# Optimization experiments

Hardware: AMD Instinct MI355X
Metric: run time of the kernel (lower is better)

Reference implementation:

```python
import jax, jax.numpy as jnp
import numpy as np

B, N, F_IN = 4, 8000, 256
D_DIST = 128   # distance_dim
DFF = 128      # hidden width of both FFNs
BIN_SIZE = 500
NBINS = N // BIN_SIZE  # 16
K = 8          # num_neighbors
DIST_MULT = 0.1
MAX_NUM_BINS = 200


def setup_inputs() -> dict:
    key = jax.random.key(0)
    ks = jax.random.split(key, 8)
    s = 0.05
    return {
        "inputs": jax.random.normal(ks[0], (B, N, F_IN), jnp.float32),
        "enc_w1": jax.random.normal(ks[1], (F_IN, DFF), jnp.float32) * s,
        "enc_b1": jnp.zeros((DFF,), jnp.float32),
        "enc_w2": jax.random.normal(ks[2], (DFF, D_DIST), jnp.float32) * s,
        "enc_b2": jnp.zeros((D_DIST,), jnp.float32),
        "edge_w1": jax.random.normal(ks[3], (2 * F_IN + 1, DFF), jnp.float32) * s,
        "edge_b1": jnp.zeros((DFF,), jnp.float32),
        "edge_w2": jax.random.normal(ks[4], (DFF, 1), jnp.float32) * s,
        "edge_b2": jnp.zeros((1,), jnp.float32),
        "rot": jax.random.normal(ks[5], (D_DIST, MAX_NUM_BINS // 2), jnp.float32) * 0.05,
    }


def _per_batch(points, rot):
    # points: [N, D_DIST]. LSH bucketing via random rotations.
    mul = points @ rot[:, : NBINS // 2]                 # [N, NBINS//2]
    cmul = jnp.concatenate([mul, -mul], axis=-1)        # [N, NBINS]
    bin_idx = jnp.argmax(cmul, axis=-1)
    bins_split = jnp.argsort(bin_idx).astype(jnp.int32).reshape(NBINS, BIN_SIZE)
    parts = points[bins_split]                          # [NBINS, BIN_SIZE, D]
    # per-bin pairwise gaussian kernel
    na = jnp.sum(parts * parts, axis=-1)                # [NBINS, BIN_SIZE]
    d2 = na[:, :, None] - 2.0 * jnp.einsum('bnd,bmd->bnm', parts, parts) + na[:, None, :]
    dm = jnp.exp(-DIST_MULT * jnp.sqrt(jnp.maximum(d2, 1e-6)))  # [NBINS, BS, BS]
    vals, idx = jax.lax.top_k(dm, K)                    # [NBINS, BS, K]
    dst = jax.vmap(lambda b, i: b[i])(bins_split, idx)  # map in-bin idx -> global
    src = jnp.broadcast_to(bins_split[:, :, None], dst.shape)
    return src.reshape(-1), dst.reshape(-1), vals.reshape(-1), bins_split


def reference(inputs, enc_w1, enc_b1, enc_w2, enc_b2,
              edge_w1, edge_b1, edge_w2, edge_b2, rot):
    # point encoding FFN: Dense(128, elu) -> Dense(distance_dim)
    pe = jax.nn.elu(inputs @ enc_w1 + enc_b1) @ enc_w2 + enc_b2  # [B, N, D_DIST]
    src, dst, vals, bins_split = jax.vmap(_per_batch, in_axes=(0, None))(pe, rot)
    bidx = jnp.broadcast_to(jnp.arange(B, dtype=jnp.int32)[:, None], src.shape)
    src = src.reshape(-1)
    dst = dst.reshape(-1)
    vals = vals.reshape(-1)
    bidx = bidx.reshape(-1)
    # tf.sparse.reorder: canonical row-major ordering (no duplicates: top-k
    # indices are distinct per row and src is unique per neighbor slot)
    order = jnp.lexsort((dst, src, bidx))
    bidx, src, dst, vals = bidx[order], src[order], dst[order], vals[order]
    # edge network on gathered endpoint features + kernel value
    x1 = inputs[bidx, src]                               # [E, F_IN]
    x2 = inputs[bidx, dst]
    e = jnp.concatenate([x1, x2, vals[:, None]], axis=-1)  # [E, 2*F_IN+1]
    edge_vals = jax.nn.sigmoid(jax.nn.elu(e @ edge_w1 + edge_b1) @ edge_w2 + edge_b2)[:, 0]
    indices = jnp.stack([bidx, src, dst], axis=-1)       # [E, 3] sparse indices
    return indices, edge_vals, bins_split
```

## Files before the change

### kernel.cpp

```cpp
#include <hip/hip_runtime.h>
#include <math.h>

#define BB 4
#define NN 8000
#define FIN 256
#define DD 128
#define NB 16
#define BS 500
#define KK 8
#define RPB 32
#define CHUNKS (NN/RPB)
#define ETOT (BB*NN*KK)

__global__ __launch_bounds__(128) void k_encode(
    const float* __restrict__ x, const float* __restrict__ w1, const float* __restrict__ b1,
    const float* __restrict__ w2, const float* __restrict__ b2, const float* __restrict__ rot,
    float* __restrict__ pe, int* __restrict__ bin_idx, int* __restrict__ localrank,
    int* __restrict__ chunkhist)
{
  __shared__ float xs[RPB*FIN];
  __shared__ float hs[RPB*DD];
  __shared__ float ps[RPB*129];
  __shared__ float ms[RPB*9];
  __shared__ int   bl[RPB];
  const int t = threadIdx.x;
  const int blk = blockIdx.x;
  const int b = blk / CHUNKS;
  const int chunk = blk % CHUNKS;
  const int row0 = chunk * RPB;

  const float4* xg4 = (const float4*)(x + ((size_t)b*NN + row0)*FIN);
  float4* xs4 = (float4*)xs;
  #pragma unroll
  for (int i=0;i<16;i++) xs4[t + i*128] = xg4[t + i*128];
  __syncthreads();

  float acc[RPB];
  { float bias = b1[t];
    #pragma unroll
    for (int r=0;r<RPB;r++) acc[r]=bias; }
  for (int k=0;k<FIN;k++){
    float w = w1[k*DD + t];
    #pragma unroll
    for (int r=0;r<RPB;r++) acc[r] = fmaf(xs[r*FIN+k], w, acc[r]);
  }
  #pragma unroll
  for (int r=0;r<RPB;r++){ float v=acc[r]; hs[r*DD+t] = v>0.f ? v : expm1f(v); }
  __syncthreads();

  { float bias = b2[t];
    #pragma unroll
    for (int r=0;r<RPB;r++) acc[r]=bias; }
  for (int k=0;k<DD;k++){
    float w = w2[k*DD + t];
    #pragma unroll
    for (int r=0;r<RPB;r++) acc[r] = fmaf(hs[r*DD+k], w, acc[r]);
  }
  #pragma unroll
  for (int r=0;r<RPB;r++){
    float v = acc[r];
    pe[((size_t)b*NN + row0 + r)*DD + t] = v;
    ps[r*129+t] = v;
  }
  __syncthreads();

  { const int r = t>>2, m0 = t&3;
    float s0=0.f, s1=0.f;
    for (int k=0;k<DD;k++){
      float p = ps[r*129+k];
      s0 = fmaf(p, rot[k*100+m0],   s0);
      s1 = fmaf(p, rot[k*100+m0+4], s1);
    }
    ms[r*9+m0]=s0; ms[r*9+m0+4]=s1; }
  __syncthreads();

  if (t<RPB){
    float best = ms[t*9+0]; int bi=0;
    #pragma unroll
    for (int m=1;m<16;m++){
      float v = (m<8)? ms[t*9+m] : -ms[t*9+(m-8)];
      if (v>best){best=v;bi=m;}
    }
    bl[t]=bi;
    bin_idx[b*NN+row0+t]=bi;
  }
  __syncthreads();
  if (t<RPB){
    int myb=bl[t]; int rk=0;
    for (int r2=0;r2<t;r2++) rk += (bl[r2]==myb) ? 1 : 0;
    localrank[b*NN+row0+t]=rk;
  }
  if (t<NB){
    int cnt=0;
    #pragma unroll
    for (int r2=0;r2<RPB;r2++) cnt += (bl[r2]==t) ? 1 : 0;
    chunkhist[(b*CHUNKS+chunk)*NB + t] = cnt;
  }
}

__global__ __launch_bounds__(128) void k_tables(
    const float* __restrict__ x, const float* __restrict__ ew1,
    float* __restrict__ A, float* __restrict__ Bv)
{
  __shared__ float xs[RPB*FIN];
  const int t=threadIdx.x, blk=blockIdx.x;
  const int b=blk/CHUNKS, chunk=blk%CHUNKS, row0=chunk*RPB;
  const float4* xg4=(const float4*)(x+((size_t)b*NN+row0)*FIN);
  float4* xs4=(float4*)xs;
  #pragma unroll
  for (int i=0;i<16;i++) xs4[t+i*128]=xg4[t+i*128];
  __syncthreads();
  float aA[RPB], aB[RPB];
  #pragma unroll
  for (int r=0;r<RPB;r++){aA[r]=0.f;aB[r]=0.f;}
  for (int k=0;k<FIN;k++){
    float wa=ew1[k*DD+t], wb=ew1[(FIN+k)*DD+t];
    #pragma unroll
    for (int r=0;r<RPB;r++){
      float xv=xs[r*FIN+k];
      aA[r]=fmaf(xv,wa,aA[r]); aB[r]=fmaf(xv,wb,aB[r]);
    }
  }
  #pragma unroll
  for (int r=0;r<RPB;r++){
    A [((size_t)b*NN+row0+r)*DD+t]=aA[r];
    Bv[((size_t)b*NN+row0+r)*DD+t]=aB[r];
  }
}

__global__ __launch_bounds__(256) void k_scan_scatter(
    const int* __restrict__ bin_idx, const int* __restrict__ localrank,
    const int* __restrict__ chunkhist, int* __restrict__ bs, float* __restrict__ out_bins)
{
  const int b=blockIdx.x, t=threadIdx.x;
  __shared__ int cbase_s[CHUNKS*NB];
  __shared__ int tot[NB], start[NB];
  if (t<NB){
    int s=0;
    for (int c=0;c<CHUNKS;c++) s+=chunkhist[(b*CHUNKS+c)*NB+t];
    tot[t]=s;
  }
  __syncthreads();
  if (t==0){
    int run=0;
    for (int m=0;m<NB;m++){ start[m]=run; run+=tot[m]; }
  }
  __syncthreads();
  if (t<NB){
    int run=start[t];
    for (int c=0;c<CHUNKS;c++){
      cbase_s[c*NB+t]=run;
      run+=chunkhist[(b*CHUNKS+c)*NB+t];
    }
  }
  __syncthreads();
  for (int row=t; row<NN; row+=256){
    int gi=b*NN+row;
    int chunk=row>>5;
    int bi=bin_idx[gi];
    int pos=cbase_s[chunk*NB+bi]+localrank[gi];
    bs[b*NN+pos]=row;
    out_bins[b*NN+pos]=(float)row;
  }
}

__global__ __launch_bounds__(256) void k_nn(
    const float* __restrict__ pe, const int* __restrict__ bs,
    float* __restrict__ out_idx, int* __restrict__ e_dst, float* __restrict__ e_val)
{
  __shared__ float RT[64*129];
  __shared__ float CT[64*129];
  __shared__ float na_all[512];
  __shared__ int   bsl[BS];
  const int t=threadIdx.x;
  const int blk=blockIdx.x;
  const int rt=blk&7, bin=(blk>>3)&15, b=blk>>7;

  for (int i=t;i<BS;i+=256) bsl[i]=bs[b*NN + bin*BS + i];
  __syncthreads();

  for (int i=t;i<BS;i+=256){
    const float* pr = pe + ((size_t)b*NN + bsl[i])*DD;
    float s=0.f;
    for (int k=0;k<DD;k+=4){
      float4 v=*(const float4*)(pr+k);
      s=fmaf(v.x,v.x,s); s=fmaf(v.y,v.y,s); s=fmaf(v.z,v.z,s); s=fmaf(v.w,v.w,s);
    }
    na_all[i]=s;
  }

  const int r0=rt*64;
  const int nr=min(64, BS-r0);
  { const int lr=t>>5, c4=t&31;
    #pragma unroll
    for (int pass=0;pass<8;pass++){
      int r=pass*8+lr;
      float4 v=make_float4(0.f,0.f,0.f,0.f);
      if (r<nr) v=*(const float4*)(pe + ((size_t)b*NN + bsl[r0+r])*DD + c4*4);
      float* d=&RT[r*129 + c4*4];
      d[0]=v.x;d[1]=v.y;d[2]=v.z;d[3]=v.w;
    } }

  float tv[4][8]; int tix[4][8];
  #pragma unroll
  for (int i=0;i<4;i++){
    #pragma unroll
    for (int s=0;s<8;s++){ tv[i][s]=-1e30f; tix[i][s]=0; } }

  const int tr_=t>>4, tc_=t&15;

  for (int ct=0; ct<8; ++ct){
    __syncthreads();
    const int c0=ct*64;
    const int nc=min(64, BS-c0);
    { const int lr=t>>5, c4=t&31;
      #pragma unroll
      for (int pass=0;pass<8;pass++){
        int c=pass*8+lr;
        float4 v=make_float4(0.f,0.f,0.f,0.f);
        if (c<nc) v=*(const float4*)(pe + ((size_t)b*NN + bsl[c0+c])*DD + c4*4);
        float* d=&CT[c*129 + c4*4];
        d[0]=v.x;d[1]=v.y;d[2]=v.z;d[3]=v.w;
      } }
    __syncthreads();

    float accm[4][4];
    #pragma unroll
    for (int i=0;i<4;i++){
      #pragma unroll
      for (int j=0;j<4;j++) accm[i][j]=0.f; }
    for (int k2=0;k2<DD;k2++){
      float av[4], bv[4];
      #pragma unroll
      for (int i=0;i<4;i++) av[i]=RT[(tr_*4+i)*129+k2];
      #pragma unroll
      for (int j=0;j<4;j++) bv[j]=CT[(tc_*4+j)*129+k2];
      #pragma unroll
      for (int i=0;i<4;i++){
        #pragma unroll
        for (int j=0;j<4;j++) accm[i][j]=fmaf(av[i],bv[j],accm[i][j]); }
    }

    float nrow[4], ncol[4];
    #pragma unroll
    for (int i=0;i<4;i++) nrow[i]=na_all[r0+tr_*4+i];
    #pragma unroll
    for (int j=0;j<4;j++) ncol[j]=na_all[c0+tc_*4+j];

    #pragma unroll
    for (int i=0;i<4;i++){
      #pragma unroll
      for (int j=0;j<4;j++){
        float t1=nrow[i]-2.f*accm[i][j];
        float d2v=t1+ncol[j];
        float dm=expf(-0.1f*sqrtf(fmaxf(d2v,1e-6f)));
        int c=c0+tc_*4+j;
        if (c<BS && dm>tv[i][7]){
          tv[i][7]=dm; tix[i][7]=c;
          #pragma unroll
          for (int q=7;q>0;q--){
            if (tv[i][q]>tv[i][q-1]){
              float tf=tv[i][q];tv[i][q]=tv[i][q-1];tv[i][q-1]=tf;
              int   td=tix[i][q];tix[i][q]=tix[i][q-1];tix[i][q-1]=td;
            }
          }
        }
      }
    }
  }

  __syncthreads();
  #pragma unroll
  for (int i=0;i<4;i++){
    const int row=tr_*4+i;
    #pragma unroll
    for (int s=0;s<8;s++){
      RT[row*129 + tc_*8 + s]=tv[i][s];
      CT[row*129 + tc_*8 + s]=__int_as_float(tix[i][s]);
    }
  }
  __syncthreads();

  if (t<nr){
    float mv[8]; int mi[8];
    #pragma unroll
    for (int s=0;s<8;s++){ mv[s]=-1e30f; mi[s]=0; }
    for (int p=0;p<128;p++){
      float v=RT[t*129+p]; int c=__float_as_int(CT[t*129+p]);
      if (v>mv[7] || (v==mv[7] && c<mi[7])){
        mv[7]=v; mi[7]=c;
        #pragma unroll
        for (int q=7;q>0;q--){
          bool sw=(mv[q]>mv[q-1]) || (mv[q]==mv[q-1] && mi[q]<mi[q-1]);
          if (sw){
            float tf=mv[q];mv[q]=mv[q-1];mv[q-1]=tf;
            int   td=mi[q];mi[q]=mi[q-1];mi[q-1]=td;
          }
        }
      }
    }
    const int src=bsl[r0+t];
    int dsts[KK]; float vv[KK];
    #pragma unroll
    for (int k2=0;k2<KK;k2++){ dsts[k2]=bsl[mi[k2]]; vv[k2]=mv[k2]; }
    #define CSWAP(a_,b_) { if (dsts[a_]>dsts[b_]){ int td=dsts[a_];dsts[a_]=dsts[b_];dsts[b_]=td; float tf=vv[a_];vv[a_]=vv[b_];vv[b_]=tf; } }
    CSWAP(0,1) CSWAP(2,3) CSWAP(4,5) CSWAP(6,7)
    CSWAP(0,2) CSWAP(1,3) CSWAP(4,6) CSWAP(5,7)
    CSWAP(1,2) CSWAP(5,6)
    CSWAP(0,4) CSWAP(1,5) CSWAP(2,6) CSWAP(3,7)
    CSWAP(2,4) CSWAP(3,5)
    CSWAP(1,2) CSWAP(3,4) CSWAP(5,6)
    #undef CSWAP
    size_t e0=((size_t)b*NN + src)*KK;
    #pragma unroll
    for (int k2=0;k2<KK;k2++){
      out_idx[3*(e0+k2)+0]=(float)b;
      out_idx[3*(e0+k2)+1]=(float)src;
      out_idx[3*(e0+k2)+2]=(float)dsts[k2];
      e_dst[e0+k2]=dsts[k2];
      e_val[e0+k2]=vv[k2];
    }
  }
}

__global__ __launch_bounds__(256) void k_edge(
    const float* __restrict__ A, const float* __restrict__ Bv,
    const float* __restrict__ ew1, const float* __restrict__ eb1,
    const float* __restrict__ ew2, const float* __restrict__ eb2,
    const int* __restrict__ e_dst, const float* __restrict__ e_val,
    float* __restrict__ out_vals)
{
  const int wid = (int)((blockIdx.x*256u+threadIdx.x)>>6);
  const int lane = threadIdx.x&63;
  if (wid >= BB*NN) return;
  const int b = wid / NN;
  const float2 a2  = *(const float2*)(A   + (size_t)wid*DD + lane*2);
  const float2 wc  = *(const float2*)(ew1 + (size_t)512*DD + lane*2);
  const float2 bb1 = *(const float2*)(eb1 + lane*2);
  const float2 w2v = *(const float2*)(ew2 + lane*2);
  const float  b2s = eb2[0];
  const size_t e0 = (size_t)wid*KK;
  #pragma unroll
  for (int k=0;k<KK;k++){
    int dst = e_dst[e0+k];
    float val = e_val[e0+k];
    const float2 bv = *(const float2*)(Bv + ((size_t)b*NN+dst)*DD + lane*2);
    float h0 = a2.x + bv.x + val*wc.x + bb1.x;  h0 = h0>0.f ? h0 : expm1f(h0);
    float h1 = a2.y + bv.y + val*wc.y + bb1.y;  h1 = h1>0.f ? h1 : expm1f(h1);
    float s = h0*w2v.x + h1*w2v.y;
    #pragma unroll
    for (int off=32; off; off>>=1) s += __shfl_xor(s, off);
    if (lane==k) out_vals[e0+k] = 1.f/(1.f+expf(-(s+b2s)));
  }
}

extern "C" void kernel_launch(void* const* d_in, const int* in_sizes, int n_in,
                              void* d_out, int out_size, void* d_ws, size_t ws_size,
                              hipStream_t stream)
{
  const float* x    = (const float*)d_in[0];
  const float* ew1v = (const float*)d_in[1];
  const float* eb1v = (const float*)d_in[2];
  const float* ew2v = (const float*)d_in[3];
  const float* eb2v = (const float*)d_in[4];
  const float* gw1  = (const float*)d_in[5];
  const float* gb1  = (const float*)d_in[6];
  const float* gw2  = (const float*)d_in[7];
  const float* gb2  = (const float*)d_in[8];
  const float* rot  = (const float*)d_in[9];

  char* w = (char*)d_ws;
  float* pe   = (float*)w;  w += (size_t)BB*NN*DD*4;
  float* Atab = (float*)w;  w += (size_t)BB*NN*DD*4;
  float* Btab = (float*)w;  w += (size_t)BB*NN*DD*4;
  int*   bin_idx   = (int*)w; w += (size_t)BB*NN*4;
  int*   localrank = (int*)w; w += (size_t)BB*NN*4;
  int*   chunkhist = (int*)w; w += (size_t)BB*CHUNKS*NB*4;
  int*   bs        = (int*)w; w += (size_t)BB*NN*4;
  int*   e_dst     = (int*)w; w += (size_t)ETOT*4;
  float* e_val     = (float*)w; w += (size_t)ETOT*4;

  float* out_idx  = (float*)d_out;
  float* out_vals = out_idx + (size_t)ETOT*3;
  float* out_bins = out_vals + ETOT;

  k_encode<<<dim3(BB*CHUNKS), dim3(128), 0, stream>>>(
      x, ew1v, eb1v, ew2v, eb2v, rot, pe, bin_idx, localrank, chunkhist);
  k_tables<<<dim3(BB*CHUNKS), dim3(128), 0, stream>>>(x, gw1, Atab, Btab);
  k_scan_scatter<<<dim3(BB), dim3(256), 0, stream>>>(
      bin_idx, localrank, chunkhist, bs, out_bins);
  k_nn<<<dim3(BB*NB*8), dim3(256), 0, stream>>>(pe, bs, out_idx, e_dst, e_val);
  k_edge<<<dim3(BB*NN/4), dim3(256), 0, stream>>>(
      Atab, Btab, gw1, gb1, gw2, gb2, e_dst, e_val, out_vals);
}
```

Baseline: 585.2 us.

## Register-tile encoder and table GEMMs; vectorize swizzled LDS reads in kNN

The encoder and edge-table kernels now use a 4x8 register tile per thread, with weights staged through shared memory in 32-row slabs. This replaces the old scheme of one column per thread with 32 rows of accumulators and a scalar global weight load on every k. The kNN distance kernel pads its tiles to a stride of 132 and reads float4 vectors from LDS, using an XOR swizzle on the column tile to avoid bank conflicts. The aim is to cut LDS and global load instructions per FMA, at the cost of more syncthreads and more shared memory per block, which may lower occupancy.

```diff
diff --git a/kernel.cpp b/kernel.cpp
--- a/kernel.cpp
+++ b/kernel.cpp
@@ -18,56 +18,126 @@
     float* __restrict__ pe, int* __restrict__ bin_idx, int* __restrict__ localrank,
     int* __restrict__ chunkhist)
 {
-  __shared__ float xs[RPB*FIN];
-  __shared__ float hs[RPB*DD];
-  __shared__ float ps[RPB*129];
+  __shared__ float xs[RPB*260];
+  __shared__ float ws[32*132];
+  __shared__ float hs[RPB*132];
   __shared__ float ms[RPB*9];
   __shared__ int   bl[RPB];
   const int t = threadIdx.x;
-  const int blk = blockIdx.x;
-  const int b = blk / CHUNKS;
-  const int chunk = blk % CHUNKS;
+  const int b = blockIdx.x / CHUNKS;
+  const int chunk = blockIdx.x % CHUNKS;
   const int row0 = chunk * RPB;
-
-  const float4* xg4 = (const float4*)(x + ((size_t)b*NN + row0)*FIN);
-  float4* xs4 = (float4*)xs;
-  #pragma unroll
-  for (int i=0;i<16;i++) xs4[t + i*128] = xg4[t + i*128];
-  __syncthreads();
-
-  float acc[RPB];
-  { float bias = b1[t];
-    #pragma unroll
-    for (int r=0;r<RPB;r++) acc[r]=bias; }
-  for (int k=0;k<FIN;k++){
-    float w = w1[k*DD + t];
-    #pragma unroll
-    for (int r=0;r<RPB;r++) acc[r] = fmaf(xs[r*FIN+k], w, acc[r]);
-  }
-  #pragma unroll
-  for (int r=0;r<RPB;r++){ float v=acc[r]; hs[r*DD+t] = v>0.f ? v : expm1f(v); }
-  __syncthreads();
-
-  { float bias = b2[t];
-    #pragma unroll
-    for (int r=0;r<RPB;r++) acc[r]=bias; }
-  for (int k=0;k<DD;k++){
-    float w = w2[k*DD + t];
-    #pragma unroll
-    for (int r=0;r<RPB;r++) acc[r] = fmaf(hs[r*DD+k], w, acc[r]);
-  }
-  #pragma unroll
-  for (int r=0;r<RPB;r++){
-    float v = acc[r];
-    pe[((size_t)b*NN + row0 + r)*DD + t] = v;
-    ps[r*129+t] = v;
-  }
+  const int ri = t >> 4;
+  const int ci = t & 15;
+
+  { const float4* xg4 = (const float4*)(x + ((size_t)b*NN + row0)*FIN);
+    #pragma unroll
+    for (int p=0;p<16;p++){
+      int idx4 = t + p*128;
+      int r = idx4 >> 6, c4 = idx4 & 63;
+      *(float4*)&xs[r*260 + c4*4] = xg4[idx4];
+    } }
+
+  float acc[4][8];
+  #pragma unroll
+  for (int i=0;i<4;i++){
+    #pragma unroll
+    for (int j=0;j<8;j++) acc[i][j] = b1[ci*8+j]; }
+  __syncthreads();
+
+  for (int kt=0; kt<8; ++kt){
+    { const float4* wg = (const float4*)(w1 + (size_t)kt*32*DD);
+      #pragma unroll
+      for (int p=0;p<8;p++){
+        int idx4 = t + p*128;
+        int k = idx4 >> 5, c4 = idx4 & 31;
+        *(float4*)&ws[k*132 + c4*4] = wg[idx4];
+      } }
+    __syncthreads();
+    #pragma unroll
+    for (int kc=0; kc<32; kc+=4){
+      float4 a4[4];
+      #pragma unroll
+      for (int i=0;i<4;i++) a4[i] = *(const float4*)&xs[(ri*4+i)*260 + kt*32 + kc];
+      #pragma unroll
+      for (int kk=0; kk<4; kk++){
+        float4 wlo = *(const float4*)&ws[(kc+kk)*132 + ci*8];
+        float4 whi = *(const float4*)&ws[(kc+kk)*132 + ci*8 + 4];
+        #pragma unroll
+        for (int i=0;i<4;i++){
+          float av = ((const float*)&a4[i])[kk];
+          acc[i][0]=fmaf(av,wlo.x,acc[i][0]); acc[i][1]=fmaf(av,wlo.y,acc[i][1]);
+          acc[i][2]=fmaf(av,wlo.z,acc[i][2]); acc[i][3]=fmaf(av,wlo.w,acc[i][3]);
+          acc[i][4]=fmaf(av,whi.x,acc[i][4]); acc[i][5]=fmaf(av,whi.y,acc[i][5]);
+          acc[i][6]=fmaf(av,whi.z,acc[i][6]); acc[i][7]=fmaf(av,whi.w,acc[i][7]);
+        }
+      }
+    }
+    __syncthreads();
+  }
+
+  #pragma unroll
+  for (int i=0;i<4;i++){
+    int r = ri*4+i;
+    #pragma unroll
+    for (int j=0;j<8;j++){
+      float v = acc[i][j];
+      hs[r*132 + ci*8 + j] = v>0.f ? v : expm1f(v);
+    } }
+  __syncthreads();
+
+  float acc2[4][8];
+  #pragma unroll
+  for (int i=0;i<4;i++){
+    #pragma unroll
+    for (int j=0;j<8;j++) acc2[i][j] = b2[ci*8+j]; }
+  for (int kt=0; kt<4; ++kt){
+    { const float4* wg = (const float4*)(w2 + (size_t)kt*32*DD);
+      #pragma unroll
+      for (int p=0;p<8;p++){
+        int idx4 = t + p*128;
+        int k = idx4 >> 5, c4 = idx4 & 31;
+        *(float4*)&ws[k*132 + c4*4] = wg[idx4];
+      } }
+    __syncthreads();
+    #pragma unroll
+    for (int kc=0; kc<32; kc+=4){
+      float4 a4[4];
+      #pragma unroll
+      for (int i=0;i<4;i++) a4[i] = *(const float4*)&hs[(ri*4+i)*132 + kt*32 + kc];
+      #pragma unroll
+      for (int kk=0; kk<4; kk++){
+        float4 wlo = *(const float4*)&ws[(kc+kk)*132 + ci*8];
+        float4 whi = *(const float4*)&ws[(kc+kk)*132 + ci*8 + 4];
+        #pragma unroll
+        for (int i=0;i<4;i++){
+          float av = ((const float*)&a4[i])[kk];
+          acc2[i][0]=fmaf(av,wlo.x,acc2[i][0]); acc2[i][1]=fmaf(av,wlo.y,acc2[i][1]);
+          acc2[i][2]=fmaf(av,wlo.z,acc2[i][2]); acc2[i][3]=fmaf(av,wlo.w,acc2[i][3]);
+          acc2[i][4]=fmaf(av,whi.x,acc2[i][4]); acc2[i][5]=fmaf(av,whi.y,acc2[i][5]);
+          acc2[i][6]=fmaf(av,whi.z,acc2[i][6]); acc2[i][7]=fmaf(av,whi.w,acc2[i][7]);
+        }
+      }
+    }
+    __syncthreads();
+  }
+
+  #pragma unroll
+  for (int i=0;i<4;i++){
+    int r = ri*4+i;
+    float* pg = pe + ((size_t)b*NN + row0 + r)*DD + ci*8;
+    #pragma unroll
+    for (int j=0;j<8;j+=4){
+      float4 v = make_float4(acc2[i][j],acc2[i][j+1],acc2[i][j+2],acc2[i][j+3]);
+      *(float4*)(pg + j) = v;
+      *(float4*)&hs[r*132 + ci*8 + j] = v;
+    } }
   __syncthreads();
 
   { const int r = t>>2, m0 = t&3;
     float s0=0.f, s1=0.f;
     for (int k=0;k<DD;k++){
-      float p = ps[r*129+k];
+      float p = hs[r*132+k];
       s0 = fmaf(p, rot[k*100+m0],   s0);
       s1 = fmaf(p, rot[k*100+m0+4], s1);
     }
@@ -102,30 +172,77 @@
     const float* __restrict__ x, const float* __restrict__ ew1,
     float* __restrict__ A, float* __restrict__ Bv)
 {
-  __shared__ float xs[RPB*FIN];
+  __shared__ float xs[RPB*260];
+  __shared__ float wsa[32*132];
+  __shared__ float wsb[32*132];
   const int t=threadIdx.x, blk=blockIdx.x;
   const int b=blk/CHUNKS, chunk=blk%CHUNKS, row0=chunk*RPB;
-  const float4* xg4=(const float4*)(x+((size_t)b*NN+row0)*FIN);
-  float4* xs4=(float4*)xs;
-  #pragma unroll
-  for (int i=0;i<16;i++) xs4[t+i*128]=xg4[t+i*128];
-  __syncthreads();
-  float aA[RPB], aB[RPB];
-  #pragma unroll
-  for (int r=0;r<RPB;r++){aA[r]=0.f;aB[r]=0.f;}
-  for (int k=0;k<FIN;k++){
-    float wa=ew1[k*DD+t], wb=ew1[(FIN+k)*DD+t];
-    #pragma unroll
-    for (int r=0;r<RPB;r++){
-      float xv=xs[r*FIN+k];
-      aA[r]=fmaf(xv,wa,aA[r]); aB[r]=fmaf(xv,wb,aB[r]);
-    }
-  }
-  #pragma unroll
-  for (int r=0;r<RPB;r++){
-    A [((size_t)b*NN+row0+r)*DD+t]=aA[r];
-    Bv[((size_t)b*NN+row0+r)*DD+t]=aB[r];
-  }
+  const int ri = t >> 4, ci = t & 15;
+
+  { const float4* xg4=(const float4*)(x+((size_t)b*NN+row0)*FIN);
+    #pragma unroll
+    for (int p=0;p<16;p++){
+      int idx4 = t + p*128;
+      int r = idx4 >> 6, c4 = idx4 & 63;
+      *(float4*)&xs[r*260 + c4*4] = xg4[idx4];
+    } }
+
+  float aA[4][8], aB[4][8];
+  #pragma unroll
+  for (int i=0;i<4;i++){
+    #pragma unroll
+    for (int j=0;j<8;j++){ aA[i][j]=0.f; aB[i][j]=0.f; } }
+  __syncthreads();
+
+  for (int kt=0; kt<8; ++kt){
+    { const float4* wga = (const float4*)(ew1 + (size_t)kt*32*DD);
+      const float4* wgb = (const float4*)(ew1 + (size_t)(FIN + kt*32)*DD);
+      #pragma unroll
+      for (int p=0;p<8;p++){
+        int idx4 = t + p*128;
+        int k = idx4 >> 5, c4 = idx4 & 31;
+        *(float4*)&wsa[k*132 + c4*4] = wga[idx4];
+        *(float4*)&wsb[k*132 + c4*4] = wgb[idx4];
+      } }
+    __syncthreads();
+    #pragma unroll 4
+    for (int kc=0; kc<32; kc+=4){
+      float4 a4[4];
+      #pragma unroll
+      for (int i=0;i<4;i++) a4[i] = *(const float4*)&xs[(ri*4+i)*260 + kt*32 + kc];
+      #pragma unroll
+      for (int kk=0; kk<4; kk++){
+        float4 alo = *(const float4*)&wsa[(kc+kk)*132 + ci*8];
+        float4 ahi = *(const float4*)&wsa[(kc+kk)*132 + ci*8 + 4];
+        float4 blo = *(const float4*)&wsb[(kc+kk)*132 + ci*8];
+        float4 bhi = *(const float4*)&wsb[(kc+kk)*132 + ci*8 + 4];
+        #pragma unroll
+        for (int i=0;i<4;i++){
+          float av = ((const float*)&a4[i])[kk];
+          aA[i][0]=fmaf(av,alo.x,aA[i][0]); aA[i][1]=fmaf(av,alo.y,aA[i][1]);
+          aA[i][2]=fmaf(av,alo.z,aA[i][2]); aA[i][3]=fmaf(av,alo.w,aA[i][3]);
+          aA[i][4]=fmaf(av,ahi.x,aA[i][4]); aA[i][5]=fmaf(av,ahi.y,aA[i][5]);
+          aA[i][6]=fmaf(av,ahi.z,aA[i][6]); aA[i][7]=fmaf(av,ahi.w,aA[i][7]);
+          aB[i][0]=fmaf(av,blo.x,aB[i][0]); aB[i][1]=fmaf(av,blo.y,aB[i][1]);
+          aB[i][2]=fmaf(av,blo.z,aB[i][2]); aB[i][3]=fmaf(av,blo.w,aB[i][3]);
+          aB[i][4]=fmaf(av,bhi.x,aB[i][4]); aB[i][5]=fmaf(av,bhi.y,aB[i][5]);
+          aB[i][6]=fmaf(av,bhi.z,aB[i][6]); aB[i][7]=fmaf(av,bhi.w,aB[i][7]);
+        }
+      }
+    }
+    __syncthreads();
+  }
+
+  #pragma unroll
+  for (int i=0;i<4;i++){
+    int r = ri*4+i;
+    float* Ag = A  + ((size_t)b*NN+row0+r)*DD + ci*8;
+    float* Bg = Bv + ((size_t)b*NN+row0+r)*DD + ci*8;
+    #pragma unroll
+    for (int j=0;j<8;j+=4){
+      *(float4*)(Ag+j) = make_float4(aA[i][j],aA[i][j+1],aA[i][j+2],aA[i][j+3]);
+      *(float4*)(Bg+j) = make_float4(aB[i][j],aB[i][j+1],aB[i][j+2],aB[i][j+3]);
+    } }
 }
 
 __global__ __launch_bounds__(256) void k_scan_scatter(
@@ -168,8 +285,8 @@
     const float* __restrict__ pe, const int* __restrict__ bs,
     float* __restrict__ out_idx, int* __restrict__ e_dst, float* __restrict__ e_val)
 {
-  __shared__ float RT[64*129];
-  __shared__ float CT[64*129];
+  __shared__ float RT[64*132];
+  __shared__ float CT[64*132];
   __shared__ float na_all[512];
   __shared__ int   bsl[BS];
   const int t=threadIdx.x;
@@ -197,8 +314,7 @@
       int r=pass*8+lr;
       float4 v=make_float4(0.f,0.f,0.f,0.f);
       if (r<nr) v=*(const float4*)(pe + ((size_t)b*NN + bsl[r0+r])*DD + c4*4);
-      float* d=&RT[r*129 + c4*4];
-      d[0]=v.x;d[1]=v.y;d[2]=v.z;d[3]=v.w;
+      *(float4*)&RT[r*132 + c4*4] = v;
     } }
 
   float tv[4][8]; int tix[4][8];
@@ -208,6 +324,7 @@
     for (int s=0;s<8;s++){ tv[i][s]=-1e30f; tix[i][s]=0; } }
 
   const int tr_=t>>4, tc_=t&15;
+  const int cswz = ((tc_>>1)&3)<<2;
 
   for (int ct=0; ct<8; ++ct){
     __syncthreads();
@@ -219,8 +336,8 @@
         int c=pass*8+lr;
         float4 v=make_float4(0.f,0.f,0.f,0.f);
         if (c<nc) v=*(const float4*)(pe + ((size_t)b*NN + bsl[c0+c])*DD + c4*4);
-        float* d=&CT[c*129 + c4*4];
-        d[0]=v.x;d[1]=v.y;d[2]=v.z;d[3]=v.w;
+        int swz = ((c>>3)&3)<<2;
+        *(float4*)&CT[c*132 + ((c4*4) ^ swz)] = v;
       } }
     __syncthreads();
 
@@ -229,16 +346,26 @@
     for (int i=0;i<4;i++){
       #pragma unroll
       for (int j=0;j<4;j++) accm[i][j]=0.f; }
-    for (int k2=0;k2<DD;k2++){
-      float av[4], bv[4];
-      #pragma unroll
-      for (int i=0;i<4;i++) av[i]=RT[(tr_*4+i)*129+k2];
-      #pragma unroll
-      for (int j=0;j<4;j++) bv[j]=CT[(tc_*4+j)*129+k2];
-      #pragma unroll
-      for (int i=0;i<4;i++){
+
+    #pragma unroll 8
+    for (int k0=0;k0<DD;k0+=4){
+      float4 a4[4], b4[4];
+      #pragma unroll
+      for (int i=0;i<4;i++) a4[i]=*(const float4*)&RT[(tr_*4+i)*132 + k0];
+      #pragma unroll
+      for (int j=0;j<4;j++) b4[j]=*(const float4*)&CT[(tc_*4+j)*132 + (k0 ^ cswz)];
+      #pragma unroll
+      for (int kk=0;kk<4;kk++){
         #pragma unroll
-        for (int j=0;j<4;j++) accm[i][j]=fmaf(av[i],bv[j],accm[i][j]); }
+        for (int i=0;i<4;i++){
+          float av=((const float*)&a4[i])[kk];
+          #pragma unroll
+          for (int j=0;j<4;j++){
+            float bvv=((const float*)&b4[j])[kk];
+            accm[i][j]=fmaf(av,bvv,accm[i][j]);
+          }
+        }
+      }
     }
 
     float nrow[4], ncol[4];
@@ -275,8 +402,8 @@
     const int row=tr_*4+i;
     #pragma unroll
     for (int s=0;s<8;s++){
-      RT[row*129 + tc_*8 + s]=tv[i][s];
-      CT[row*129 + tc_*8 + s]=__int_as_float(tix[i][s]);
+      RT[row*132 + tc_*8 + s]=tv[i][s];
+      CT[row*132 + tc_*8 + s]=__int_as_float(tix[i][s]);
     }
   }
   __syncthreads();
@@ -286,7 +413,7 @@
     #pragma unroll
     for (int s=0;s<8;s++){ mv[s]=-1e30f; mi[s]=0; }
     for (int p=0;p<128;p++){
-      float v=RT[t*129+p]; int c=__float_as_int(CT[t*129+p]);
+      float v=RT[t*132+p]; int c=__float_as_int(CT[t*132+p]);
       if (v>mv[7] || (v==mv[7] && c<mi[7])){
         mv[7]=v; mi[7]=c;
         #pragma unroll
```

Result: faster. 529.7 us (-9.5%).
